# Performance work log

Measured on AMD Instinct MI355X. Metric: run time of the kernel, lower is better.

## Reference

```python
import jax, jax.numpy as jnp
import numpy as np
from jax import lax

B, S, D = 4, 2048, 512          # batch, doc seq len, input_size
Y = 8922                          # num labels (ICD codes)
V, E = 50000, 100                 # vocab, word embed dim
T, K = 32, 9                      # code-title tokens, conv filter size
PAD = K // 2


def setup_inputs() -> dict:
    key = jax.random.key(0)
    ks = jax.random.split(key, 8)
    x = jax.random.normal(ks[0], (B, S, D), dtype=jnp.float32)
    target = jax.random.randint(ks[1], (B, Y), 0, 2).astype(jnp.float32)
    c2title = jax.random.randint(ks[2], (Y, T), 0, V)
    embed_W = jax.random.normal(ks[3], (V, E), dtype=jnp.float32) * 0.1
    conv_w = jax.random.normal(ks[4], (D, E, K), dtype=jnp.float32) * 0.05  # [out, in, k]
    conv_b = jax.random.normal(ks[5], (D,), dtype=jnp.float32) * 0.05
    final_w = jax.random.normal(ks[6], (Y, D), dtype=jnp.float32) * 0.05
    final_b = jax.random.normal(ks[7], (Y,), dtype=jnp.float32) * 0.05
    return {"x": x, "target": target, "c2title": c2title, "embed_W": embed_W,
            "conv_w": conv_w, "conv_b": conv_b, "final_w": final_w, "final_b": final_b}


def reference(x, target, c2title, embed_W, conv_w, conv_b, final_w, final_b):
    # Code-title encoder: embed -> Conv1d (same padding) -> max-pool over time -> tanh
    ct = embed_W[c2title]                      # [Y, T, E]
    ct = jnp.transpose(ct, (0, 2, 1))          # [Y, E, T]  (NCH)
    U = lax.conv_general_dilated(ct, conv_w, window_strides=(1,),
                                 padding=[(PAD, PAD)],
                                 dimension_numbers=("NCH", "OIH", "NCH"))
    U = U + conv_b[None, :, None]              # [Y, D, T]
    U = jnp.tanh(jnp.max(U, axis=-1))          # [Y, D]  (MaxPool1d(T) + tanh)

    # Label cross-attention over document tokens
    scale = 1.0 / jnp.sqrt(jnp.float32(D))
    scores = jnp.einsum("yd,bsd->bys", U, x) * scale   # [B, Y, S]
    alpha = jax.nn.softmax(scores, axis=-1)             # softmax over seq
    m = jnp.einsum("bys,bsd->byd", alpha, x)            # [B, Y, D]

    # Per-label elementwise dot product + bias
    y = jnp.einsum("byd,yd->by", m, final_w) + final_b  # [B, Y]

    # BCEWithLogitsLoss (mean), numerically stable
    loss = jnp.mean(jnp.maximum(y, 0.0) - y * target + jnp.log1p(jnp.exp(-jnp.abs(y))))
    return (y, loss, alpha, m)
```

## Files before the change

kernel.cpp:

```cpp
#include <hip/hip_runtime.h>
#include <math.h>

#define BQ 4
#define SQ 2048
#define DQ 512
#define YQ 8922
#define TQ 32
#define EQ 100
#define EP 128
#define KQ 9
#define LD 128
#define TP 40
#define YPAD 8960

typedef float f32x4 __attribute__((ext_vector_type(4)));
typedef short s16x8 __attribute__((ext_vector_type(8)));

static __device__ __forceinline__ f32x4 mfma16(s16x8 a, s16x8 b, f32x4 c) {
  return __builtin_amdgcn_mfma_f32_16x16x32_bf16(a, b, c, 0, 0, 0);
}

static __device__ __forceinline__ ushort f2bf(float f) {
  union { float f; unsigned u; } v; v.f = f;
  unsigned r = (v.u + 0x7FFFu + ((v.u >> 16) & 1u)) >> 16;
  return (ushort)r;
}

static __device__ __forceinline__ float bf2f(ushort h) {
  union { unsigned u; float f; } v; v.u = ((unsigned)h) << 16; return v.f;
}

static __device__ __forceinline__ f32x4 ld4u(const float* p) {
  f32x4 v; __builtin_memcpy(&v, p, 16); return v;
}

static __device__ __forceinline__ int swz_chunk(int row, int chunk) {
  return chunk ^ (row & 15);
}
static __device__ __forceinline__ int swz3(int row, int chunk) {
  return chunk ^ (row & 7);
}

__global__ void k_prep_x(const float* __restrict__ x, ushort* __restrict__ xb,
                         ushort* __restrict__ xT) {
  __shared__ ushort sm[32][33];
  int b = blockIdx.z;
  int s0 = blockIdx.x * 32;
  int d0 = blockIdx.y * 32;
  int tx = threadIdx.x, ty = threadIdx.y;
  float v = x[((size_t)b * SQ + s0 + ty) * DQ + d0 + tx];
  ushort h = f2bf(v);
  xb[((size_t)b * SQ + s0 + ty) * DQ + d0 + tx] = h;
  sm[ty][tx] = h;
  __syncthreads();
  xT[((size_t)b * DQ + d0 + ty) * SQ + s0 + tx] = sm[tx][ty];
}

__global__ void k_pack_w(const float* __restrict__ cw, ushort* __restrict__ Wp) {
  int i = blockIdx.x * 256 + threadIdx.x;
  if (i >= KQ * DQ * EP) return;
  int e = i & (EP - 1);
  int d = (i >> 7) & (DQ - 1);
  int kk = i >> 16;
  float v = (e < EQ) ? cw[((size_t)d * EQ + e) * KQ + kk] : 0.f;
  Wp[i] = f2bf(v);
}

__launch_bounds__(256, 2)
__global__ void k_conv(const int* __restrict__ c2t, const float* __restrict__ embed,
                       const ushort* __restrict__ Wp, const float* __restrict__ cb,
                       ushort* __restrict__ U) {
  __shared__ ushort sA[4 * TP * LD];
  __shared__ ushort sB[128 * LD];
  const f32x4 fz4 = {0.f, 0.f, 0.f, 0.f};
  int tid = threadIdx.x;
  int d0 = blockIdx.x * 128;
  int y0 = blockIdx.y * 4;
  int lane = tid & 63, wave = tid >> 6;
  int wm = wave & 1, wn = wave >> 1;
  int lr = lane & 15, lg = lane >> 4;

  #pragma unroll
  for (int it = 0; it < 2; ++it) {
    int u = tid + it * 256;
    if (u < 2 * 4 * TP) {
      int row = u >> 1, half = u & 1;
      int yl = row / TP, tt = row - yl * TP;
      int ts = tt - 4;
      int y = y0 + yl;
      const float* src = 0;
      if (y < YQ && (unsigned)ts < (unsigned)TQ)
        src = embed + (size_t)c2t[y * TQ + ts] * EQ + half * 64;
      #pragma unroll
      for (int j = 0; j < 16; ++j) {
        int col = half * 64 + j * 4;
        f32x4 v = fz4;
        if (src != 0 && col + 4 <= EQ) v = *(const f32x4*)(src + j * 4);
        ushort4 h = make_ushort4(f2bf(v.x), f2bf(v.y), f2bf(v.z), f2bf(v.w));
        int pc = swz_chunk(row, col >> 3);
        *(ushort4*)&sA[row * LD + pc * 8 + (col & 7)] = h;
      }
    }
  }

  s16x8 breg[8];
  {
    const ushort* src = Wp + (size_t)d0 * EP;
    #pragma unroll
    for (int it = 0; it < 8; ++it) {
      int gi = tid + it * 256, r = gi >> 4, g = gi & 15;
      breg[it] = *(const s16x8*)(src + (size_t)r * EP + g * 8);
    }
    #pragma unroll
    for (int it = 0; it < 8; ++it) {
      int gi = tid + it * 256, r = gi >> 4, g = gi & 15;
      *(s16x8*)&sB[r * LD + swz_chunk(r, g) * 8] = breg[it];
    }
  }
  __syncthreads();

  f32x4 acc[4][4];
  #pragma unroll
  for (int i = 0; i < 4; ++i)
    #pragma unroll
    for (int j = 0; j < 4; ++j) acc[i][j] = fz4;

  for (int kk = 0; kk < KQ; ++kk) {
    if (kk + 1 < KQ) {
      const ushort* src = Wp + ((size_t)(kk + 1) * DQ + d0) * EP;
      #pragma unroll
      for (int it = 0; it < 8; ++it) {
        int gi = tid + it * 256, r = gi >> 4, g = gi & 15;
        breg[it] = *(const s16x8*)(src + (size_t)r * EP + g * 8);
      }
    }
    #pragma unroll
    for (int ee = 0; ee < 4; ++ee) {
      s16x8 af[4], bfr[4];
      #pragma unroll
      for (int i = 0; i < 4; ++i) {
        int rowm = wm * 64 + i * 16 + lr;
        int yl = rowm >> 5;
        int row = yl * TP + (rowm & 31) + kk;
        af[i] = *(const s16x8*)&sA[row * LD + swz_chunk(row, ee * 4 + lg) * 8];
      }
      #pragma unroll
      for (int i = 0; i < 4; ++i) {
        int row = wn * 64 + i * 16 + lr;
        bfr[i] = *(const s16x8*)&sB[row * LD + swz_chunk(row, ee * 4 + lg) * 8];
      }
      #pragma unroll
      for (int i = 0; i < 4; ++i)
        #pragma unroll
        for (int j = 0; j < 4; ++j)
          acc[i][j] = mfma16(af[i], bfr[j], acc[i][j]);
    }
    __syncthreads();
    if (kk + 1 < KQ) {
      #pragma unroll
      for (int it = 0; it < 8; ++it) {
        int gi = tid + it * 256, r = gi >> 4, g = gi & 15;
        *(s16x8*)&sB[r * LD + swz_chunk(r, g) * 8] = breg[it];
      }
      __syncthreads();
    }
  }

  const float scl = 0.04419417382415922f;
  #pragma unroll
  for (int L2 = 0; L2 < 2; ++L2) {
    int y = y0 + wm * 2 + L2;
    #pragma unroll
    for (int j = 0; j < 4; ++j) {
      float mx = -3.0e38f;
      #pragma unroll
      for (int ii = 0; ii < 2; ++ii)
        #pragma unroll
        for (int q = 0; q < 4; ++q)
          mx = fmaxf(mx, acc[L2 * 2 + ii][j][q]);
      mx = fmaxf(mx, __shfl_xor(mx, 16));
      mx = fmaxf(mx, __shfl_xor(mx, 32));
      if (lane < 16 && y < YQ) {
        int col = d0 + wn * 64 + j * 16 + lane;
        U[(size_t)y * DQ + col] = f2bf(tanhf(mx + cb[col]) * scl);
      }
    }
  }
}

__launch_bounds__(256, 2)
__global__ void k_scores(const ushort* __restrict__ U, const ushort* __restrict__ xb,
                         float* __restrict__ sc, float* __restrict__ part) {
  __shared__ ushort sA[128 * LD];
  __shared__ ushort sB[128 * LD];
  const f32x4 fz4 = {0.f, 0.f, 0.f, 0.f};
  int tid = threadIdx.x;
  int s0 = blockIdx.x * 128;
  int y0 = blockIdx.y * 128;
  int b = blockIdx.z;
  const ushort* Ap = U + (size_t)y0 * DQ;
  const ushort* Bp = xb + ((size_t)b * SQ + s0) * DQ;
  f32x4 acc[4][4];
  #pragma unroll
  for (int i = 0; i < 4; ++i)
    #pragma unroll
    for (int j = 0; j < 4; ++j) acc[i][j] = fz4;
  int lane = tid & 63, wave = tid >> 6;
  int wm = wave & 1, wn = wave >> 1;
  int lr = lane & 15, lg = lane >> 4;

  for (int kc = 0; kc < DQ; kc += 128) {
    __syncthreads();
    #pragma unroll
    for (int it = 0; it < 8; ++it) {
      int gi = tid + it * 256;
      int r = gi >> 4, g = gi & 15;
      int pofs = r * LD + swz_chunk(r, g) * 8;
      *(s16x8*)&sA[pofs] = *(const s16x8*)(Ap + (size_t)r * DQ + kc + g * 8);
      *(s16x8*)&sB[pofs] = *(const s16x8*)(Bp + (size_t)r * DQ + kc + g * 8);
    }
    __syncthreads();
    #pragma unroll
    for (int ks = 0; ks < 4; ++ks) {
      s16x8 af[4], bfr[4];
      #pragma unroll
      for (int i = 0; i < 4; ++i) {
        int row = wm * 64 + i * 16 + lr;
        af[i] = *(const s16x8*)&sA[row * LD + swz_chunk(row, ks * 4 + lg) * 8];
      }
      #pragma unroll
      for (int i = 0; i < 4; ++i) {
        int row = wn * 64 + i * 16 + lr;
        bfr[i] = *(const s16x8*)&sB[row * LD + swz_chunk(row, ks * 4 + lg) * 8];
      }
      #pragma unroll
      for (int i = 0; i < 4; ++i)
        #pragma unroll
        for (int j = 0; j < 4; ++j)
          acc[i][j] = mfma16(af[i], bfr[j], acc[i][j]);
    }
  }
  float* out = sc + (size_t)b * YQ * SQ;
  int rb = wm * 64 + lg * 4;
  int cb_ = wn * 64 + lr;
  #pragma unroll
  for (int i = 0; i < 4; ++i)
    #pragma unroll
    for (int j = 0; j < 4; ++j) {
      int col = s0 + cb_ + j * 16;
      #pragma unroll
      for (int q = 0; q < 4; ++q) {
        int r = y0 + rb + i * 16 + q;
        if (r < YQ) out[(size_t)r * SQ + col] = acc[i][j][q];
      }
    }

  int hb = blockIdx.x * 2 + wn;
  #pragma unroll
  for (int i = 0; i < 4; ++i)
    #pragma unroll
    for (int q = 0; q < 4; ++q) {
      float mx = fmaxf(fmaxf(acc[i][0][q], acc[i][1][q]),
                       fmaxf(acc[i][2][q], acc[i][3][q]));
      #pragma unroll
      for (int o = 1; o < 16; o <<= 1) mx = fmaxf(mx, __shfl_xor(mx, o));
      float se = 0.f;
      #pragma unroll
      for (int j = 0; j < 4; ++j) se += __expf(acc[i][j][q] - mx);
      #pragma unroll
      for (int o = 1; o < 16; o <<= 1) se += __shfl_xor(se, o);
      int r = y0 + rb + i * 16 + q;
      if (lr == 0 && r < YQ) {
        float* pp = part + ((size_t)(b * YQ + r) * 32 + hb) * 2;
        pp[0] = mx;
        pp[1] = se;
      }
    }
}

__global__ void k_smfix(const float* __restrict__ part, float* __restrict__ rs) {
  int t = blockIdx.x * 256 + threadIdx.x;
  if (t >= BQ * YQ) return;
  const float* pp = part + (size_t)t * 64;
  float M = -3.0e38f;
  #pragma unroll
  for (int h = 0; h < 32; ++h) M = fmaxf(M, pp[h * 2]);
  float Z = 0.f;
  #pragma unroll
  for (int h = 0; h < 32; ++h) Z += __expf(pp[h * 2] - M) * pp[h * 2 + 1];
  rs[t * 2] = M;
  rs[t * 2 + 1] = 1.0f / Z;
}

__global__ void k_alpha(float* __restrict__ a, const float* __restrict__ rs,
                        ushort* __restrict__ abf) {
  int r = blockIdx.x;
  float M = rs[r * 2], iZ = rs[r * 2 + 1];
  float* p = a + (size_t)r * SQ;
  int tid = threadIdx.x;
  if (abf) {
    ushort* q = abf + (size_t)r * SQ;
    #pragma unroll
    for (int i = 0; i < 8; ++i) {
      int e = tid + i * 256;
      q[e] = f2bf(__expf(p[e] - M) * iZ);
    }
  } else {
    #pragma unroll
    for (int i = 0; i < 8; ++i) {
      int e = tid + i * 256;
      p[e] = __expf(p[e] - M) * iZ;
    }
  }
}

__launch_bounds__(512, 4)
__global__ void k_pv2(const ushort* __restrict__ abf, const ushort* __restrict__ xT,
                      float* __restrict__ mo, float* __restrict__ aout) {
  __shared__ ushort sA[128 * 64];
  __shared__ ushort sB[256 * 64];
  const f32x4 fz4 = {0.f, 0.f, 0.f, 0.f};
  const s16x8 sz8 = {0, 0, 0, 0, 0, 0, 0, 0};
  int tid = threadIdx.x;
  int d0 = blockIdx.x * 256;
  int y0 = blockIdx.y * 128;
  int b = blockIdx.z;
  int lane = tid & 63, wave = tid >> 6;
  int wm = wave >> 1;
  int wn = wave & 1;
  int lr = lane & 15, lg = lane >> 4;
  bool wr_alpha = (blockIdx.x == 0);

  const ushort* Ap = abf + ((size_t)b * YQ + y0) * SQ;
  const ushort* Bp = xT + ((size_t)b * DQ + d0) * SQ;

  f32x4 acc[2][8];
  #pragma unroll
  for (int i = 0; i < 2; ++i)
    #pragma unroll
    for (int j = 0; j < 8; ++j) acc[i][j] = fz4;

  for (int kc = 0; kc < SQ; kc += 64) {
    #pragma unroll
    for (int p = 0; p < 2; ++p) {
      int u = tid + p * 512;
      int r = u >> 3, c = u & 7;
      int y = y0 + r;
      s16x8 v = sz8;
      if (y < YQ) {
        size_t base = (size_t)r * SQ + kc + c * 8;
        v = *(const s16x8*)(Ap + base);
        if (wr_alpha) {
          float* ao = aout + ((size_t)b * YQ + y) * SQ + kc + c * 8;
          f32x4 w0, w1;
          #pragma unroll
          for (int k2 = 0; k2 < 4; ++k2) w0[k2] = bf2f((ushort)v[k2]);
          #pragma unroll
          for (int k2 = 0; k2 < 4; ++k2) w1[k2] = bf2f((ushort)v[4 + k2]);
          *(f32x4*)ao = w0;
          *(f32x4*)(ao + 4) = w1;
        }
      }
      *(s16x8*)&sA[r * 64 + swz3(r, c) * 8] = v;
    }
    #pragma unroll
    for (int p = 0; p < 4; ++p) {
      int u = tid + p * 512;
      int r = u >> 3, c = u & 7;
      *(s16x8*)&sB[r * 64 + swz3(r, c) * 8] =
          *(const s16x8*)(Bp + (size_t)r * SQ + kc + c * 8);
    }
    __syncthreads();
    #pragma unroll
    for (int ks = 0; ks < 2; ++ks) {
      s16x8 af[2];
      #pragma unroll
      for (int i = 0; i < 2; ++i) {
        int row = wm * 32 + i * 16 + lr;
        af[i] = *(const s16x8*)&sA[row * 64 + swz3(row, ks * 4 + lg) * 8];
      }
      #pragma unroll
      for (int j = 0; j < 8; ++j) {
        int row = wn * 128 + j * 16 + lr;
        s16x8 bf = *(const s16x8*)&sB[row * 64 + swz3(row, ks * 4 + lg) * 8];
        acc[0][j] = mfma16(af[0], bf, acc[0][j]);
        acc[1][j] = mfma16(af[1], bf, acc[1][j]);
      }
    }
    __syncthreads();
  }

  float* out = mo + (size_t)b * YQ * DQ;
  #pragma unroll
  for (int i = 0; i < 2; ++i)
    #pragma unroll
    for (int q = 0; q < 4; ++q) {
      int r = y0 + wm * 32 + i * 16 + lg * 4 + q;
      if (r >= YQ) continue;
      #pragma unroll
      for (int j = 0; j < 8; ++j) {
        int col = d0 + wn * 128 + j * 16 + lr;
        out[(size_t)r * DQ + col] = acc[i][j][q];
      }
    }
}

__launch_bounds__(256, 2)
__global__ void k_pv(const float* __restrict__ alpha, const ushort* __restrict__ xT,
                     float* __restrict__ mo) {
  __shared__ ushort sA[128 * LD];
  __shared__ ushort sB[128 * LD];
  const f32x4 fz4 = {0.f, 0.f, 0.f, 0.f};
  int tid = threadIdx.x;
  int d0 = blockIdx.x * 128;
  int y0 = blockIdx.y * 128;
  int b = blockIdx.z;
  const float* Ap = alpha + ((size_t)b * YQ + y0) * SQ;
  const ushort* Bp = xT + ((size_t)b * DQ + d0) * SQ;
  f32x4 acc[4][4];
  #pragma unroll
  for (int i = 0; i < 4; ++i)
    #pragma unroll
    for (int j = 0; j < 4; ++j) acc[i][j] = fz4;
  int lane = tid & 63, wave = tid >> 6;
  int wm = wave & 1, wn = wave >> 1;
  int lr = lane & 15, lg = lane >> 4;

  for (int kc = 0; kc < SQ; kc += 128) {
    __syncthreads();
    #pragma unroll
    for (int it = 0; it < 8; ++it) {
      int gi = tid + it * 256;
      int r = gi >> 4, g = gi & 15;
      int y = y0 + r;
      int pofs = r * LD + swz_chunk(r, g) * 8;
      ushort4 h0 = make_ushort4(0, 0, 0, 0), h1 = make_ushort4(0, 0, 0, 0);
      if (y < YQ) {
        f32x4 v0 = ld4u(Ap + (size_t)r * SQ + kc + g * 8);
        f32x4 v1 = ld4u(Ap + (size_t)r * SQ + kc + g * 8 + 4);
        h0 = make_ushort4(f2bf(v0.x), f2bf(v0.y), f2bf(v0.z), f2bf(v0.w));
        h1 = make_ushort4(f2bf(v1.x), f2bf(v1.y), f2bf(v1.z), f2bf(v1.w));
      }
      *(ushort4*)&sA[pofs] = h0;
      *(ushort4*)&sA[pofs + 4] = h1;
      *(s16x8*)&sB[pofs] = *(const s16x8*)(Bp + (size_t)r * SQ + kc + g * 8);
    }
    __syncthreads();
    #pragma unroll
    for (int ks = 0; ks < 4; ++ks) {
      s16x8 af[4], bfr[4];
      #pragma unroll
      for (int i = 0; i < 4; ++i) {
        int row = wm * 64 + i * 16 + lr;
        af[i] = *(const s16x8*)&sA[row * LD + swz_chunk(row, ks * 4 + lg) * 8];
      }
      #pragma unroll
      for (int i = 0; i < 4; ++i) {
        int row = wn * 64 + i * 16 + lr;
        bfr[i] = *(const s16x8*)&sB[row * LD + swz_chunk(row, ks * 4 + lg) * 8];
      }
      #pragma unroll
      for (int i = 0; i < 4; ++i)
        #pragma unroll
        for (int j = 0; j < 4; ++j)
          acc[i][j] = mfma16(af[i], bfr[j], acc[i][j]);
    }
  }
  float* out = mo + (size_t)b * YQ * DQ;
  int rb = wm * 64 + lg * 4;
  int cb_ = wn * 64 + lr;
  #pragma unroll
  for (int i = 0; i < 4; ++i)
    #pragma unroll
    for (int j = 0; j < 4; ++j) {
      int col = d0 + cb_ + j * 16;
      #pragma unroll
      for (int q = 0; q < 4; ++q) {
        int r = y0 + rb + i * 16 + q;
        if (r < YQ) out[(size_t)r * DQ + col] = acc[i][j][q];
      }
    }
}

__global__ void k_final(const float* __restrict__ m_in, const float* __restrict__ fw,
                        const float* __restrict__ fb, const float* __restrict__ tgt,
                        float* __restrict__ yo, float* __restrict__ part) {
  int y = blockIdx.x;
  int lane = threadIdx.x & 63;
  int b = threadIdx.x >> 6;
  const float* mp = m_in + ((size_t)b * YQ + y) * DQ;
  const float* wp = fw + (size_t)y * DQ;
  float s = 0.f;
  #pragma unroll
  for (int i = 0; i < 8; ++i) {
    int e = lane + i * 64;
    s += mp[e] * wp[e];
  }
  #pragma unroll
  for (int o = 32; o > 0; o >>= 1) s += __shfl_xor(s, o);
  __shared__ float pl[4];
  if (lane == 0) {
    float yv = s + fb[y];
    yo[(size_t)b * YQ + y] = yv;
    float t = tgt[(size_t)b * YQ + y];
    pl[b] = fmaxf(yv, 0.f) - yv * t + log1pf(__expf(-fabsf(yv)));
  }
  __syncthreads();
  if (threadIdx.x == 0)
    part[y] = (pl[0] + pl[1]) + (pl[2] + pl[3]);
}

__global__ void k_loss_fin(const float* __restrict__ part, float* __restrict__ out) {
  int tid = threadIdx.x;
  float s = 0.f;
  for (int i = tid; i < YQ; i += 256) s += part[i];
  #pragma unroll
  for (int o = 32; o > 0; o >>= 1) s += __shfl_xor(s, o);
  __shared__ float red[4];
  int lane = tid & 63, wave = tid >> 6;
  if (lane == 0) red[wave] = s;
  __syncthreads();
  if (tid == 0)
    out[0] = ((red[0] + red[1]) + (red[2] + red[3])) * (1.0f / (float)(BQ * YQ));
}

extern "C" void kernel_launch(void* const* d_in, const int* in_sizes, int n_in,
                              void* d_out, int out_size, void* d_ws, size_t ws_size,
                              hipStream_t stream) {
  const float* x      = (const float*)d_in[0];
  const float* target = (const float*)d_in[1];
  const int*   c2t    = (const int*)d_in[2];
  const float* embed  = (const float*)d_in[3];
  const float* cw     = (const float*)d_in[4];
  const float* cb     = (const float*)d_in[5];
  const float* fw     = (const float*)d_in[6];
  const float* fb     = (const float*)d_in[7];

  char* ws = (char*)d_ws;
  ushort* xb   = (ushort*)(ws);
  ushort* xT   = (ushort*)(ws + 8388608);
  ushort* Wp   = (ushort*)(ws + 16777216);
  ushort* U    = (ushort*)(ws + 17956864);
  float* lpart = (float*)(ws + 27131904);
  float* part  = (float*)(ws + 27167744);
  float* rst   = (float*)(ws + 36303872);
  const size_t ABF_OFF = 36589568;
  const size_t NEED_ABF = ABF_OFF + (size_t)BQ * YQ * SQ * 2;
  bool use_abf = (ws_size >= NEED_ABF);
  ushort* abf = use_abf ? (ushort*)(ws + ABF_OFF) : (ushort*)0;

  float* out       = (float*)d_out;
  float* out_y     = out;
  float* out_loss  = out + (size_t)BQ * YQ;
  float* out_alpha = out + (size_t)BQ * YQ + 1;
  float* out_m     = out_alpha + (size_t)BQ * YQ * SQ;

  hipMemsetAsync(U, 0, (size_t)YPAD * DQ * 2, stream);

  k_prep_x<<<dim3(SQ / 32, DQ / 32, BQ), dim3(32, 32), 0, stream>>>(x, xb, xT);
  k_pack_w<<<dim3((KQ * DQ * EP + 255) / 256), 256, 0, stream>>>(cw, Wp);
  k_conv<<<dim3(4, (YQ + 3) / 4), 256, 0, stream>>>(c2t, embed, Wp, cb, U);
  k_scores<<<dim3(SQ / 128, (YQ + 127) / 128, BQ), 256, 0, stream>>>(U, xb, out_alpha, part);
  k_smfix<<<dim3((BQ * YQ + 255) / 256), 256, 0, stream>>>(part, rst);
  k_alpha<<<dim3(BQ * YQ), 256, 0, stream>>>(out_alpha, rst, abf);
  if (use_abf)
    k_pv2<<<dim3(DQ / 256, (YQ + 127) / 128, BQ), 512, 0, stream>>>(abf, xT, out_m, out_alpha);
  else
    k_pv<<<dim3(DQ / 128, (YQ + 127) / 128, BQ), 256, 0, stream>>>(out_alpha, xT, out_m);
  k_final<<<dim3(YQ), 256, 0, stream>>>(out_m, fw, fb, target, out_y, lpart);
  k_loss_fin<<<1, 256, 0, stream>>>(lpart, out_loss);
}
```

Measured before the change: 997.8 us.

## Vectorize prep/alpha kernels, drop conv padding rows, split alpha write across blocks

Rewrites the x transpose/convert kernel to use 64x64 tiles with float4 loads and ushort4 stores. Vectorizes the softmax-normalize kernel to 4-wide loads and stores. Removes the padded rows from the conv shared tile, zero-filling out-of-range taps in registers instead. Spreads the fp32 alpha output write in k_pv2 across both d-blocks by sequence half rather than having one block write it all. Together these aim to reduce memory instruction count and balance store traffic, at the cost of extra branching in the conv inner loop.

```diff
diff --git a/kernel.cpp b/kernel.cpp
--- a/kernel.cpp
+++ b/kernel.cpp
@@ -10,7 +10,6 @@
 #define EP 128
 #define KQ 9
 #define LD 128
-#define TP 40
 #define YPAD 8960
 
 typedef float f32x4 __attribute__((ext_vector_type(4)));
@@ -33,6 +32,9 @@
 static __device__ __forceinline__ f32x4 ld4u(const float* p) {
   f32x4 v; __builtin_memcpy(&v, p, 16); return v;
 }
+static __device__ __forceinline__ void st4u(float* p, f32x4 v) {
+  __builtin_memcpy(p, &v, 16);
+}
 
 static __device__ __forceinline__ int swz_chunk(int row, int chunk) {
   return chunk ^ (row & 15);
@@ -43,17 +45,29 @@
 
 __global__ void k_prep_x(const float* __restrict__ x, ushort* __restrict__ xb,
                          ushort* __restrict__ xT) {
-  __shared__ ushort sm[32][33];
+  __shared__ ushort sm[64][66];
   int b = blockIdx.z;
-  int s0 = blockIdx.x * 32;
-  int d0 = blockIdx.y * 32;
-  int tx = threadIdx.x, ty = threadIdx.y;
-  float v = x[((size_t)b * SQ + s0 + ty) * DQ + d0 + tx];
-  ushort h = f2bf(v);
-  xb[((size_t)b * SQ + s0 + ty) * DQ + d0 + tx] = h;
-  sm[ty][tx] = h;
+  int s0 = blockIdx.x * 64;
+  int d0 = blockIdx.y * 64;
+  int tid = threadIdx.x;
+  int sr = tid >> 4;
+  int c4 = (tid & 15) * 4;
+  #pragma unroll
+  for (int it = 0; it < 4; ++it) {
+    int s = sr + it * 16;
+    f32x4 v = *(const f32x4*)(x + ((size_t)b * SQ + s0 + s) * DQ + d0 + c4);
+    ushort4 h = make_ushort4(f2bf(v.x), f2bf(v.y), f2bf(v.z), f2bf(v.w));
+    *(ushort4*)(xb + ((size_t)b * SQ + s0 + s) * DQ + d0 + c4) = h;
+    sm[s][c4] = h.x; sm[s][c4 + 1] = h.y; sm[s][c4 + 2] = h.z; sm[s][c4 + 3] = h.w;
+  }
   __syncthreads();
-  xT[((size_t)b * DQ + d0 + ty) * SQ + s0 + tx] = sm[tx][ty];
+  #pragma unroll
+  for (int it = 0; it < 4; ++it) {
+    int d = sr + it * 16;
+    ushort4 h;
+    h.x = sm[c4][d]; h.y = sm[c4 + 1][d]; h.z = sm[c4 + 2][d]; h.w = sm[c4 + 3][d];
+    *(ushort4*)(xT + ((size_t)b * DQ + d0 + d) * SQ + s0 + c4) = h;
+  }
 }
 
 __global__ void k_pack_w(const float* __restrict__ cw, ushort* __restrict__ Wp) {
@@ -70,9 +84,10 @@
 __global__ void k_conv(const int* __restrict__ c2t, const float* __restrict__ embed,
                        const ushort* __restrict__ Wp, const float* __restrict__ cb,
                        ushort* __restrict__ U) {
-  __shared__ ushort sA[4 * TP * LD];
+  __shared__ ushort sA[4 * TQ * LD];
   __shared__ ushort sB[128 * LD];
   const f32x4 fz4 = {0.f, 0.f, 0.f, 0.f};
+  const s16x8 sz8 = {0, 0, 0, 0, 0, 0, 0, 0};
   int tid = threadIdx.x;
   int d0 = blockIdx.x * 128;
   int y0 = blockIdx.y * 4;
@@ -80,26 +95,21 @@
   int wm = wave & 1, wn = wave >> 1;
   int lr = lane & 15, lg = lane >> 4;
 
-  #pragma unroll
-  for (int it = 0; it < 2; ++it) {
-    int u = tid + it * 256;
-    if (u < 2 * 4 * TP) {
-      int row = u >> 1, half = u & 1;
-      int yl = row / TP, tt = row - yl * TP;
-      int ts = tt - 4;
-      int y = y0 + yl;
-      const float* src = 0;
-      if (y < YQ && (unsigned)ts < (unsigned)TQ)
-        src = embed + (size_t)c2t[y * TQ + ts] * EQ + half * 64;
-      #pragma unroll
-      for (int j = 0; j < 16; ++j) {
-        int col = half * 64 + j * 4;
-        f32x4 v = fz4;
-        if (src != 0 && col + 4 <= EQ) v = *(const f32x4*)(src + j * 4);
-        ushort4 h = make_ushort4(f2bf(v.x), f2bf(v.y), f2bf(v.z), f2bf(v.w));
-        int pc = swz_chunk(row, col >> 3);
-        *(ushort4*)&sA[row * LD + pc * 8 + (col & 7)] = h;
-      }
+  {
+    int row = tid >> 1;
+    int half = tid & 1;
+    int yl = row >> 5, t = row & 31;
+    int y = y0 + yl;
+    const float* src = 0;
+    if (y < YQ) src = embed + (size_t)c2t[y * TQ + t] * EQ + half * 64;
+    #pragma unroll
+    for (int j = 0; j < 16; ++j) {
+      int col = half * 64 + j * 4;
+      f32x4 v = fz4;
+      if (src != 0 && col + 4 <= EQ) v = *(const f32x4*)(src + j * 4);
+      ushort4 h = make_ushort4(f2bf(v.x), f2bf(v.y), f2bf(v.z), f2bf(v.w));
+      int pc = swz_chunk(row, col >> 3);
+      *(ushort4*)&sA[row * LD + pc * 8 + (col & 7)] = h;
     }
   }
 
@@ -141,8 +151,13 @@
       for (int i = 0; i < 4; ++i) {
         int rowm = wm * 64 + i * 16 + lr;
         int yl = rowm >> 5;
-        int row = yl * TP + (rowm & 31) + kk;
-        af[i] = *(const s16x8*)&sA[row * LD + swz_chunk(row, ee * 4 + lg) * 8];
+        int ts = (rowm & 31) + kk - 4;
+        s16x8 a = sz8;
+        if ((unsigned)ts < (unsigned)TQ) {
+          int row = yl * TQ + ts;
+          a = *(const s16x8*)&sA[row * LD + swz_chunk(row, ee * 4 + lg) * 8];
+        }
+        af[i] = a;
       }
       #pragma unroll
       for (int i = 0; i < 4; ++i) {
@@ -301,15 +316,26 @@
   if (abf) {
     ushort* q = abf + (size_t)r * SQ;
     #pragma unroll
-    for (int i = 0; i < 8; ++i) {
-      int e = tid + i * 256;
-      q[e] = f2bf(__expf(p[e] - M) * iZ);
+    for (int i = 0; i < 2; ++i) {
+      int e = (tid + i * 256) * 4;
+      f32x4 v = ld4u(p + e);
+      ushort4 h;
+      h.x = f2bf(__expf(v.x - M) * iZ);
+      h.y = f2bf(__expf(v.y - M) * iZ);
+      h.z = f2bf(__expf(v.z - M) * iZ);
+      h.w = f2bf(__expf(v.w - M) * iZ);
+      *(ushort4*)(q + e) = h;
     }
   } else {
     #pragma unroll
-    for (int i = 0; i < 8; ++i) {
-      int e = tid + i * 256;
-      p[e] = __expf(p[e] - M) * iZ;
+    for (int i = 0; i < 2; ++i) {
+      int e = (tid + i * 256) * 4;
+      f32x4 v = ld4u(p + e);
+      v.x = __expf(v.x - M) * iZ;
+      v.y = __expf(v.y - M) * iZ;
+      v.z = __expf(v.z - M) * iZ;
+      v.w = __expf(v.w - M) * iZ;
+      st4u(p + e, v);
     }
   }
 }
@@ -329,7 +355,6 @@
   int wm = wave >> 1;
   int wn = wave & 1;
   int lr = lane & 15, lg = lane >> 4;
-  bool wr_alpha = (blockIdx.x == 0);
 
   const ushort* Ap = abf + ((size_t)b * YQ + y0) * SQ;
   const ushort* Bp = xT + ((size_t)b * DQ + d0) * SQ;
@@ -341,6 +366,7 @@
     for (int j = 0; j < 8; ++j) acc[i][j] = fz4;
 
   for (int kc = 0; kc < SQ; kc += 64) {
+    bool wr_alpha = ((kc >> 10) == (int)blockIdx.x);
     #pragma unroll
     for (int p = 0; p < 2; ++p) {
       int u = tid + p * 512;
@@ -357,8 +383,8 @@
           for (int k2 = 0; k2 < 4; ++k2) w0[k2] = bf2f((ushort)v[k2]);
           #pragma unroll
           for (int k2 = 0; k2 < 4; ++k2) w1[k2] = bf2f((ushort)v[4 + k2]);
-          *(f32x4*)ao = w0;
-          *(f32x4*)(ao + 4) = w1;
+          st4u(ao, w0);
+          st4u(ao + 4, w1);
         }
       }
       *(s16x8*)&sA[r * 64 + swz3(r, c) * 8] = v;
@@ -557,7 +583,7 @@
 
   hipMemsetAsync(U, 0, (size_t)YPAD * DQ * 2, stream);
 
-  k_prep_x<<<dim3(SQ / 32, DQ / 32, BQ), dim3(32, 32), 0, stream>>>(x, xb, xT);
+  k_prep_x<<<dim3(SQ / 64, DQ / 64, BQ), 256, 0, stream>>>(x, xb, xT);
   k_pack_w<<<dim3((KQ * DQ * EP + 255) / 256), 256, 0, stream>>>(cw, Wp);
   k_conv<<<dim3(4, (YQ + 3) / 4), 256, 0, stream>>>(c2t, embed, Wp, cb, U);
   k_scores<<<dim3(SQ / 128, (YQ + 127) / 128, BQ), 256, 0, stream>>>(U, xb, out_alpha, part);
```

After: 935.8 us. 1.07x faster.
